# Kernel optimization log

Hardware: AMD Instinct MI355X
Metric: run time of the kernel (lower is better)

The kernel has to match this reference:

```python
import jax, jax.numpy as jnp
import numpy as np

C = 16       # celltypes
N = 20000    # nodes per PPI graph
D = 192      # in_channels == out_channels*heads (residual constraint)
H = 3        # node_heads
CO = 64      # out_channels per head
E = 320000   # edges per PPI graph
T = 32       # tissue nodes
K = 8        # neighbors per tissue
M = C + T    # metagraph nodes
R = 4        # metagraph relations
EM = 256     # edges per metagraph relation
S = 128      # sem_att_channels
TU = 100     # tissue_update iterations


def setup_inputs():
    key = jax.random.key(0)
    k = jax.random.split(key, 16)
    g = lambda kk, shp, sc: jax.random.normal(kk, shp, jnp.float32) * sc
    return {
        "ppi_x": g(k[0], (C, N, D), 1.0),
        "metagraph_x": g(k[1], (M, D), 1.0),
        "ppi_lin": g(k[2], (C, D, H * CO), 0.07),
        "ppi_att_src": g(k[3], (C, H, CO), 0.1),
        "ppi_att_dst": g(k[4], (C, H, CO), 0.1),
        "ppi_bias": jnp.zeros((C, H * CO), jnp.float32),
        "meta_lin": g(k[5], (R, H * CO, H * CO), 0.07),
        "meta_att_src": g(k[6], (R, H, CO), 0.1),
        "meta_att_dst": g(k[7], (R, H, CO), 0.1),
        "meta_bias": jnp.zeros((R, H * CO), jnp.float32),
        "W_sem": g(k[8], (H * CO, S), 0.08),
        "b_sem": jnp.zeros((S,), jnp.float32),
        "q_sem": g(k[9], (S,), 0.1),
        "ppi_edges": jax.random.randint(k[10], (C, 2, E), 0, N, dtype=jnp.int32),
        "meta_edges": jax.random.randint(k[11], (R, 2, EM), 0, M, dtype=jnp.int32),
        "tissue_nb": jax.random.randint(k[12], (T, K), 0, M, dtype=jnp.int32),
    }


def gat(x, lin, att_s, att_d, bias, edge, n):
    """PyG-style GATConv, concat heads. x:[n,Din], edge:[2,E] (src,dst)."""
    h = (x @ lin).reshape(n, H, CO)
    a_s = (h * att_s).sum(-1)   # [n,H]
    a_d = (h * att_d).sum(-1)
    src, dst = edge[0], edge[1]
    e = jax.nn.leaky_relu(a_s[src] + a_d[dst], negative_slope=0.2)  # [E,H]
    emax = jax.lax.stop_gradient(jax.ops.segment_max(e, dst, num_segments=n))
    emax = jnp.where(jnp.isfinite(emax), emax, 0.0)
    ex = jnp.exp(e - emax[dst])
    denom = jax.ops.segment_sum(ex, dst, num_segments=n)          # [n,H]
    out = jax.ops.segment_sum(ex[:, :, None] * h[src], dst, num_segments=n)
    out = out / jnp.where(denom > 0.0, denom, 1.0)[:, :, None]
    return out.reshape(n, H * CO) + bias


def sem_attention(out, W, b, q):
    """Semantic attention over relations. out:[M,R,Dh]."""
    w = jnp.tanh(jnp.einsum('mrd,ds->mrs', out, W) + b)
    beta = jax.nn.softmax(jnp.einsum('mrs,s->mr', w, q), axis=1)
    return jnp.einsum('mrd,mr->md', out, beta)


def forward(ppi_x, metagraph_x, ppi_lin, ppi_att_src, ppi_att_dst, ppi_bias,
            meta_lin, meta_att_src, meta_att_dst, meta_bias,
            W_sem, b_sem, q_sem, ppi_edges, meta_edges, tissue_nb):
    mx = metagraph_x
    # residual GAT per celltype, mean-pooled into the metagraph celltype row
    for c in range(C):
        att = ppi_x[c] + gat(ppi_x[c], ppi_lin[c], ppi_att_src[c], ppi_att_dst[c],
                             ppi_bias[c], ppi_edges[c], N)
        mx = mx.at[c].add(att.mean(0))
    # sequential (Gauss-Seidel) tissue-neighbor mean diffusion, TU sweeps
    def step(m, t):
        return m.at[C + t].set(m[tissue_nb[t]].mean(0)), None
    def sweep(m, _):
        m, _ = jax.lax.scan(step, m, jnp.arange(T))
        return m, None
    mx, _ = jax.lax.scan(sweep, mx, None, length=TU)
    # multi-relation metagraph GAT + semantic attention fusion
    outs = jnp.stack([gat(mx, meta_lin[r], meta_att_src[r], meta_att_dst[r],
                          meta_bias[r], meta_edges[r], M) for r in range(R)], axis=1)
    outs = jax.nn.relu(outs)  # torch applies relu after stacking
    return sem_attention(outs, W_sem, b_sem, q_sem)


def reference(ppi_x, metagraph_x, ppi_lin, ppi_att_src, ppi_att_dst, ppi_bias,
              meta_lin, meta_att_src, meta_att_dst, meta_bias,
              W_sem, b_sem, q_sem, ppi_edges, meta_edges, tissue_nb):
    return forward(ppi_x, metagraph_x, ppi_lin, ppi_att_src, ppi_att_dst, ppi_bias,
                   meta_lin, meta_att_src, meta_att_dst, meta_bias,
                   W_sem, b_sem, q_sem, ppi_edges, meta_edges, tissue_nb)
```

## Files before the change

kernel.cpp:

```cpp
#include <hip/hip_runtime.h>

#define CT 16
#define NN 20000
#define EE 320000
#define MM 48
#define RR 4
#define EMM 256
#define NRANGE 64
#define NPR 313
#define CAP 5632
#define MAGIC 13721941ULL

#define OFF_MEANX 0
#define OFF_P     3072
#define OFF_CNTD  12288
#define OFF_CNTS  13312
#define ZERO_FLOATS 14336
#define OFF_COMB  14336
#define OFF_AS    2574336
#define OFF_AD    3854336
#define OFF_U     5134336
#define OFF_V     5143552
#define OFF_MX    5152768
#define OFF_HH    5161984
#define OFF_OUTS  5198848
#define OFF_BIND  5235712
#define OFF_BINS  11002880
#define OFF_W     16770048
#define OFF_MX2   16772352

__device__ inline unsigned bucket_of(int d) {
    return (unsigned)(((unsigned long long)(unsigned)d * MAGIC) >> 32);
}

__global__ __launch_bounds__(192) void k_prep(const float* __restrict__ lin,
        const float* __restrict__ as_g, const float* __restrict__ ad_g,
        float* __restrict__ U, float* __restrict__ V, float* __restrict__ zws) {
    int c = blockIdx.x, d = threadIdx.x;
    int gt = c * 192 + d;
    for (int o = gt; o < ZERO_FLOATS; o += 16 * 192) zws[o] = 0.f;
    const float* L  = lin + ((size_t)c * 192 + d) * 192;
    const float* As = as_g + c * 192;
    const float* Ad = ad_g + c * 192;
#pragma unroll
    for (int h = 0; h < 3; ++h) {
        float u = 0.f, v = 0.f;
        for (int j = 0; j < 64; ++j) {
            float lv = L[h * 64 + j];
            u += lv * As[h * 64 + j];
            v += lv * Ad[h * 64 + j];
        }
        U[c * 576 + h * 192 + d] = u;
        V[c * 576 + h * 192 + d] = v;
    }
}

__global__ __launch_bounds__(256, 8) void k_front(const int* __restrict__ edges,
        int* __restrict__ cntD, int* __restrict__ cntS,
        int* __restrict__ binD, int* __restrict__ binS,
        const float* __restrict__ x, const float* __restrict__ U,
        const float* __restrict__ V, float* __restrict__ a_s,
        float* __restrict__ a_d, float* __restrict__ meanx,
        const int* __restrict__ nb, float* __restrict__ Wout) {
    __shared__ __align__(16) float smem[4608];
    int tid = threadIdx.x;
    if (blockIdx.x == 0) {
        float* B0 = smem;
        float* B1 = smem + 1536;
        float* B2 = smem + 3072;
        float* B[3] = {B0, B1, B2};
        for (int o = tid; o < 1536; o += 256) {
            int i = o / 48, j = o - i * 48;
            float idv = (j == 16 + i) ? 1.f : 0.f;
            B0[o] = idv;
            B1[o] = idv;
        }
        __syncthreads();
        if (tid < 48) {
            int j = tid;
            for (int t = 0; t < 32; ++t) {
                float acc = 0.f;
                for (int k = 0; k < 8; ++k) {
                    int idx = nb[t * 8 + k];
                    acc += (idx < 16) ? (j == idx ? 1.f : 0.f)
                                      : B0[(idx - 16) * 48 + j];
                }
                B0[t * 48 + j] = acc * 0.125f;
            }
        }
        __syncthreads();
        int iP = 0, iR = 1, iT = 2;
        int e = 100;
        while (e) {
            if (e & 1) {
                for (int o = tid; o < 1536; o += 256) {
                    int i = o / 48, j = o - i * 48;
                    float acc = (j < 16) ? B[iR][i * 48 + j] : 0.f;
                    for (int t = 0; t < 32; ++t)
                        acc += B[iR][i * 48 + 16 + t] * B[iP][t * 48 + j];
                    B[iT][o] = acc;
                }
                __syncthreads();
                int t_ = iR; iR = iT; iT = t_;
            }
            e >>= 1;
            if (e) {
                for (int o = tid; o < 1536; o += 256) {
                    int i = o / 48, j = o - i * 48;
                    float acc = (j < 16) ? B[iP][i * 48 + j] : 0.f;
                    for (int t = 0; t < 32; ++t)
                        acc += B[iP][i * 48 + 16 + t] * B[iP][t * 48 + j];
                    B[iT][o] = acc;
                }
                __syncthreads();
                int t_ = iP; iP = iT; iT = t_;
            }
        }
        for (int o = tid; o < 1536; o += 256) {
            int i = o / 48, j = o - i * 48;
            Wout[(16 + i) * 48 + j] = B[iR][o];
        }
    } else if (blockIdx.x < 1025) {
        int wg = blockIdx.x - 1;
        int ct = (wg & 7) * 2 + ((wg >> 3) & 1);
        int part = wg >> 4;
        int wave = tid >> 6;
        int* histD = (int*)smem;
        int* histS = histD + 256;
        int* curD  = histS + 256;
        int* curS  = curD + 64;
        if (tid < NRANGE) {
            histD[0 * 64 + tid] = 0; histD[1 * 64 + tid] = 0;
            histD[2 * 64 + tid] = 0; histD[3 * 64 + tid] = 0;
            histS[0 * 64 + tid] = 0; histS[1 * 64 + tid] = 0;
            histS[2 * 64 + tid] = 0; histS[3 * 64 + tid] = 0;
        }
        __syncthreads();
        const int* srcp = edges + (size_t)ct * 2 * EE;
        const int* dstp = srcp + EE;
        const int4* s4 = (const int4*)srcp;
        const int4* d4 = (const int4*)dstp;
        int base4 = part * 1250;
        for (int i = tid; i < 1250; i += 256) {
            int4 dv = d4[base4 + i];
            int4 sv = s4[base4 + i];
            atomicAdd(&histD[wave * 64 + bucket_of(dv.x)], 1);
            atomicAdd(&histD[wave * 64 + bucket_of(dv.y)], 1);
            atomicAdd(&histD[wave * 64 + bucket_of(dv.z)], 1);
            atomicAdd(&histD[wave * 64 + bucket_of(dv.w)], 1);
            atomicAdd(&histS[wave * 64 + bucket_of(sv.x)], 1);
            atomicAdd(&histS[wave * 64 + bucket_of(sv.y)], 1);
            atomicAdd(&histS[wave * 64 + bucket_of(sv.z)], 1);
            atomicAdd(&histS[wave * 64 + bucket_of(sv.w)], 1);
        }
        __syncthreads();
        if (tid < NRANGE) {
            int t = histD[tid] + histD[64 + tid] + histD[128 + tid] + histD[192 + tid];
            curD[tid] = atomicAdd(&cntD[ct * NRANGE + tid], t);
            int t2 = histS[tid] + histS[64 + tid] + histS[128 + tid] + histS[192 + tid];
            curS[tid] = atomicAdd(&cntS[ct * NRANGE + tid], t2);
        }
        __syncthreads();
        int* bD = binD + (size_t)ct * NRANGE * CAP;
        int* bS = binS + (size_t)ct * NRANGE * CAP;
#define EMIT2(ss, dd) { int pk = ((ss) << 15) | (dd); \
        unsigned bd = bucket_of(dd); int so = atomicAdd(&curD[bd], 1); \
        if (so < CAP) bD[bd * CAP + so] = pk; \
        unsigned bs = bucket_of(ss); int s2 = atomicAdd(&curS[bs], 1); \
        if (s2 < CAP) bS[bs * CAP + s2] = pk; }
        for (int i = tid; i < 1250; i += 256) {
            int4 dv = d4[base4 + i];
            int4 sv = s4[base4 + i];
            EMIT2(sv.x, dv.x); EMIT2(sv.y, dv.y); EMIT2(sv.z, dv.z); EMIT2(sv.w, dv.w);
        }
#undef EMIT2
    } else {
        int idx = blockIdx.x - 1025;
        int c = idx & 15;
        int start = (idx >> 4) * 160;
        int lane = tid & 63;
        int wave = tid >> 6;
        float* A = smem;
        float* blk = smem + 3264;
        if (tid < 192) blk[tid] = 0.f;
        float u0[3], u1[3], u2[3], v0[3], v1[3], v2[3];
#pragma unroll
        for (int h = 0; h < 3; ++h) {
            u0[h] = U[c * 576 + h * 192 + lane];
            u1[h] = U[c * 576 + h * 192 + 64 + lane];
            u2[h] = U[c * 576 + h * 192 + 128 + lane];
            v0[h] = V[c * 576 + h * 192 + lane];
            v1[h] = V[c * 576 + h * 192 + 64 + lane];
            v2[h] = V[c * 576 + h * 192 + 128 + lane];
        }
        __syncthreads();
        const float* xc = x + (size_t)c * NN * 192;
        float* asn = a_s + (size_t)c * NN * 4;
        float* adn = a_d + (size_t)c * NN * 4;
        float m0 = 0.f, m1 = 0.f, m2 = 0.f;
        float* Aa = A + (wave * 2) * 408;
        float* Ab = A + (wave * 2 + 1) * 408;
        int rrow = lane >> 3, seg = lane & 7;
        for (int i = 0; i < 20; ++i) {
            int na = start + wave + 8 * i;
            int nb_ = na + 4;
            const float* xa = xc + (size_t)na * 192;
            const float* xb = xc + (size_t)nb_ * 192;
            float xa0 = xa[lane], xa1 = xa[64 + lane], xa2 = xa[128 + lane];
            float xb0 = xb[lane], xb1 = xb[64 + lane], xb2 = xb[128 + lane];
            m0 += xa0 + xb0; m1 += xa1 + xb1; m2 += xa2 + xb2;
            Aa[0 * 68 + lane] = xa0 * u0[0] + xa1 * u1[0] + xa2 * u2[0];
            Aa[1 * 68 + lane] = xa0 * u0[1] + xa1 * u1[1] + xa2 * u2[1];
            Aa[2 * 68 + lane] = xa0 * u0[2] + xa1 * u1[2] + xa2 * u2[2];
            Aa[3 * 68 + lane] = xa0 * v0[0] + xa1 * v1[0] + xa2 * v2[0];
            Aa[4 * 68 + lane] = xa0 * v0[1] + xa1 * v1[1] + xa2 * v2[1];
            Aa[5 * 68 + lane] = xa0 * v0[2] + xa1 * v1[2] + xa2 * v2[2];
            Ab[0 * 68 + lane] = xb0 * u0[0] + xb1 * u1[0] + xb2 * u2[0];
            Ab[1 * 68 + lane] = xb0 * u0[1] + xb1 * u1[1] + xb2 * u2[1];
            Ab[2 * 68 + lane] = xb0 * u0[2] + xb1 * u1[2] + xb2 * u2[2];
            Ab[3 * 68 + lane] = xb0 * v0[0] + xb1 * v1[0] + xb2 * v2[0];
            Ab[4 * 68 + lane] = xb0 * v0[1] + xb1 * v1[1] + xb2 * v2[1];
            Ab[5 * 68 + lane] = xb0 * v0[2] + xb1 * v1[2] + xb2 * v2[2];
            float sa = 0.f, sb = 0.f;
            if (lane < 48) {
                const float4* pa = (const float4*)(Aa + rrow * 68 + seg * 8);
                const float4* pb = (const float4*)(Ab + rrow * 68 + seg * 8);
                float4 a0 = pa[0], a1 = pa[1];
                float4 b0 = pb[0], b1 = pb[1];
                sa = ((a0.x + a0.y) + (a0.z + a0.w)) + ((a1.x + a1.y) + (a1.z + a1.w));
                sb = ((b0.x + b0.y) + (b0.z + b0.w)) + ((b1.x + b1.y) + (b1.z + b1.w));
            }
            sa += __shfl_xor(sa, 1, 64); sb += __shfl_xor(sb, 1, 64);
            sa += __shfl_xor(sa, 2, 64); sb += __shfl_xor(sb, 2, 64);
            sa += __shfl_xor(sa, 4, 64); sb += __shfl_xor(sb, 4, 64);
            if (lane < 48 && seg == 0) {
                if (rrow < 3) { asn[na * 4 + rrow] = sa;      asn[nb_ * 4 + rrow] = sb; }
                else          { adn[na * 4 + rrow - 3] = sa;  adn[nb_ * 4 + rrow - 3] = sb; }
            }
        }
        atomicAdd(&blk[lane], m0);
        atomicAdd(&blk[64 + lane], m1);
        atomicAdd(&blk[128 + lane], m2);
        __syncthreads();
        if (tid < 192) atomicAdd(&meanx[c * 192 + tid], blk[tid]);
    }
}

__device__ inline void map_ct(int wg, int& ct, int& j) {
    int xcd = wg & 7;
    ct = xcd * 2 + ((wg >> 3) & 1);
    j = wg >> 4;
}

__global__ __launch_bounds__(512) void k_eden_b(const int* __restrict__ bin,
        const int* __restrict__ cnt, const float* __restrict__ a_s,
        const float* __restrict__ a_d, float* __restrict__ comb) {
    int ct, bkt;
    map_ct(blockIdx.x, ct, bkt);
    int lo = bkt * NPR;
    int nnode = NN - lo < NPR ? NN - lo : NPR;
    int tid = threadIdx.x;
    __shared__ float adl[NPR * 3];
    __shared__ float den[NPR * 3];
    const float4* as4 = (const float4*)(a_s + (size_t)ct * NN * 4);
    const float4* ad4 = (const float4*)(a_d + (size_t)ct * NN * 4);
    for (int m = tid; m < nnode; m += 512) {
        float4 v = ad4[lo + m];
        adl[m * 3] = v.x; adl[m * 3 + 1] = v.y; adl[m * 3 + 2] = v.z;
    }
    for (int o = tid; o < nnode * 3; o += 512) den[o] = 0.f;
    __syncthreads();
    int n = cnt[ct * NRANGE + bkt]; if (n > CAP) n = CAP;
    const int* bc = bin + ((size_t)ct * NRANGE + bkt) * CAP;
    for (int i = tid; i < n; i += 512) {
        int v = bc[i];
        int d = v & 32767, s = v >> 15;
        int dl = d - lo;
        float4 av = as4[s];
        float e0 = av.x + adl[dl * 3];     e0 = e0 >= 0.f ? e0 : 0.2f * e0;
        float e1 = av.y + adl[dl * 3 + 1]; e1 = e1 >= 0.f ? e1 : 0.2f * e1;
        float e2 = av.z + adl[dl * 3 + 2]; e2 = e2 >= 0.f ? e2 : 0.2f * e2;
        atomicAdd(&den[dl * 3],     __expf(e0));
        atomicAdd(&den[dl * 3 + 1], __expf(e1));
        atomicAdd(&den[dl * 3 + 2], __expf(e2));
    }
    __syncthreads();
    float4* cb = (float4*)(comb + (size_t)ct * NN * 8);
    for (int m = tid; m < nnode; m += 512) {
        float d0 = den[m * 3], d1 = den[m * 3 + 1], d2 = den[m * 3 + 2];
        float4 a, b;
        a.x = adl[m * 3]; a.y = adl[m * 3 + 1]; a.z = adl[m * 3 + 2]; a.w = 0.f;
        b.x = d0 > 0.f ? 1.f / d0 : 0.f;
        b.y = d1 > 0.f ? 1.f / d1 : 0.f;
        b.z = d2 > 0.f ? 1.f / d2 : 0.f;
        b.w = 0.f;
        cb[(size_t)(lo + m) * 2]     = a;
        cb[(size_t)(lo + m) * 2 + 1] = b;
    }
}

__global__ __launch_bounds__(512) void k_es_p(const int* __restrict__ bin,
        const int* __restrict__ cnt, const float* __restrict__ a_s,
        const float* __restrict__ comb, const float* __restrict__ x,
        float* __restrict__ p) {
    int ct, bkt;
    map_ct(blockIdx.x, ct, bkt);
    int lo = bkt * NPR;
    int nnode = NN - lo < NPR ? NN - lo : NPR;
    int tid = threadIdx.x;
    __shared__ float asl[NPR * 3];
    __shared__ float sl[NPR * 3];
    __shared__ float blk[576];
    const float4* as4 = (const float4*)(a_s + (size_t)ct * NN * 4);
    const float4* cb  = (const float4*)(comb + (size_t)ct * NN * 8);
    for (int m = tid; m < nnode; m += 512) {
        float4 v = as4[lo + m];
        asl[m * 3] = v.x; asl[m * 3 + 1] = v.y; asl[m * 3 + 2] = v.z;
    }
    for (int o = tid; o < nnode * 3; o += 512) sl[o] = 0.f;
    for (int o = tid; o < 576; o += 512) blk[o] = 0.f;
    __syncthreads();
    int n = cnt[ct * NRANGE + bkt]; if (n > CAP) n = CAP;
    const int* bc = bin + ((size_t)ct * NRANGE + bkt) * CAP;
    for (int i = tid; i < n; i += 512) {
        int v = bc[i];
        int d = v & 32767, s = v >> 15;
        int slc = s - lo;
        float4 av = cb[(size_t)d * 2];
        float4 dv = cb[(size_t)d * 2 + 1];
        float e0 = asl[slc * 3]     + av.x; e0 = e0 >= 0.f ? e0 : 0.2f * e0;
        float e1 = asl[slc * 3 + 1] + av.y; e1 = e1 >= 0.f ? e1 : 0.2f * e1;
        float e2 = asl[slc * 3 + 2] + av.z; e2 = e2 >= 0.f ? e2 : 0.2f * e2;
        atomicAdd(&sl[slc * 3],     __expf(e0) * dv.x);
        atomicAdd(&sl[slc * 3 + 1], __expf(e1) * dv.y);
        atomicAdd(&sl[slc * 3 + 2], __expf(e2) * dv.z);
    }
    __syncthreads();
    int lane = tid & 63;
    int wave = tid >> 6;
    const float* xc = x + (size_t)ct * NN * 192;
    float a00 = 0, a01 = 0, a02 = 0, a10 = 0, a11 = 0, a12 = 0, a20 = 0, a21 = 0, a22 = 0;
    for (int m = wave; m < nnode; m += 8) {
        float s0 = sl[m * 3], s1 = sl[m * 3 + 1], s2 = sl[m * 3 + 2];
        const float* xr = xc + (size_t)(lo + m) * 192;
        float x0 = xr[lane], x1 = xr[64 + lane], x2 = xr[128 + lane];
        a00 += s0 * x0; a01 += s0 * x1; a02 += s0 * x2;
        a10 += s1 * x0; a11 += s1 * x1; a12 += s1 * x2;
        a20 += s2 * x0; a21 += s2 * x1; a22 += s2 * x2;
    }
    atomicAdd(&blk[0 * 192 + lane], a00);
    atomicAdd(&blk[0 * 192 + 64 + lane], a01);
    atomicAdd(&blk[0 * 192 + 128 + lane], a02);
    atomicAdd(&blk[1 * 192 + lane], a10);
    atomicAdd(&blk[1 * 192 + 64 + lane], a11);
    atomicAdd(&blk[1 * 192 + 128 + lane], a12);
    atomicAdd(&blk[2 * 192 + lane], a20);
    atomicAdd(&blk[2 * 192 + 64 + lane], a21);
    atomicAdd(&blk[2 * 192 + 128 + lane], a22);
    __syncthreads();
    for (int o = tid; o < 576; o += 512) atomicAdd(&p[ct * 576 + o], blk[o]);
}

__global__ __launch_bounds__(192) void k_mx(const float* __restrict__ mgx,
        const float* __restrict__ meanx, const float* __restrict__ p,
        const float* __restrict__ lin, const float* __restrict__ bias,
        float* __restrict__ mx) {
    int m = blockIdx.x, j = threadIdx.x;
    if (m < CT) {
        int h = j >> 6;
        const float* ph = p + m * 576 + h * 192;
        const float* L = lin + (size_t)m * 36864;
        float acc = 0.f;
        for (int k = 0; k < 192; ++k) acc += ph[k] * L[k * 192 + j];
        mx[m * 192 + j] = mgx[m * 192 + j] + (meanx[m * 192 + j] + acc) * (1.f / NN)
                          + bias[m * 192 + j];
    } else {
        mx[m * 192 + j] = mgx[m * 192 + j];
    }
}

__global__ __launch_bounds__(192) void k_tapply(const float* __restrict__ W,
        const float* __restrict__ mx, float* __restrict__ mx2) {
    int m = blockIdx.x, j = threadIdx.x;
    if (m < CT) {
        mx2[m * 192 + j] = mx[m * 192 + j];
    } else {
        float acc = 0.f;
        for (int k = 0; k < 48; ++k) acc += W[m * 48 + k] * mx[k * 192 + j];
        mx2[m * 192 + j] = acc;
    }
}

__global__ __launch_bounds__(192) void k_meta_h(const float* __restrict__ mx,
        const float* __restrict__ lin, float* __restrict__ hh) {
    int r = blockIdx.x, m = blockIdx.y, j = threadIdx.x;
    const float* L = lin + (size_t)r * 36864;
    const float* xr = mx + m * 192;
    float acc = 0.f;
    for (int k = 0; k < 192; ++k) acc += xr[k] * L[k * 192 + j];
    hh[((size_t)r * 48 + m) * 192 + j] = acc;
}

__global__ __launch_bounds__(256) void k_meta_edge(const float* __restrict__ hh,
        const float* __restrict__ att_s, const float* __restrict__ att_d,
        const float* __restrict__ bias, const int* __restrict__ edges,
        float* __restrict__ outs) {
    int r = blockIdx.x;
    int tid = threadIdx.x;
    __shared__ float as_[48][3], ad_[48][3], den[48][3];
    const float* hr = hh + (size_t)r * 48 * 192;
    float* og = outs + (size_t)r * 48 * 192;
    if (tid < 144) {
        int m = tid / 3, h = tid % 3;
        const float* As = att_s + r * 192 + h * 64;
        const float* Ad = att_d + r * 192 + h * 64;
        float s_ = 0.f, d_ = 0.f;
        for (int j = 0; j < 64; ++j) {
            float hv = hr[m * 192 + h * 64 + j];
            s_ += hv * As[j]; d_ += hv * Ad[j];
        }
        as_[m][h] = s_; ad_[m][h] = d_;
        den[m][h] = 0.f;
    }
    for (int o = tid; o < 9216; o += 256) og[o] = bias[r * 192 + (o % 192)];
    __syncthreads();
    int s = edges[(size_t)r * 2 * EMM + tid];
    int d = edges[(size_t)r * 2 * EMM + EMM + tid];
    float e0 = as_[s][0] + ad_[d][0]; e0 = e0 >= 0.f ? e0 : 0.2f * e0;
    float e1 = as_[s][1] + ad_[d][1]; e1 = e1 >= 0.f ? e1 : 0.2f * e1;
    float e2 = as_[s][2] + ad_[d][2]; e2 = e2 >= 0.f ? e2 : 0.2f * e2;
    float ex0 = __expf(e0), ex1 = __expf(e1), ex2 = __expf(e2);
    atomicAdd(&den[d][0], ex0);
    atomicAdd(&den[d][1], ex1);
    atomicAdd(&den[d][2], ex2);
    __syncthreads();
    float w0 = ex0 / den[d][0], w1 = ex1 / den[d][1], w2 = ex2 / den[d][2];
    const float* hs = hr + s * 192;
    float* od = og + d * 192;
    for (int j = 0; j < 64; ++j)        atomicAdd(&od[j], w0 * hs[j]);
    for (int j = 64; j < 128; ++j)      atomicAdd(&od[j], w1 * hs[j]);
    for (int j = 128; j < 192; ++j)     atomicAdd(&od[j], w2 * hs[j]);
}

__global__ __launch_bounds__(128) void k_sem(const float* __restrict__ outs,
        const float* __restrict__ W, const float* __restrict__ b,
        const float* __restrict__ q, float* __restrict__ out) {
    int m = blockIdx.x, s = threadIdx.x;
    __shared__ float ro[4][192];
    __shared__ float red[4][128];
    __shared__ float beta[4];
    for (int o = s; o < 768; o += 128) {
        int r = o / 192, d = o - r * 192;
        float v = outs[((size_t)r * 48 + m) * 192 + d];
        ro[r][d] = v > 0.f ? v : 0.f;
    }
    __syncthreads();
    float p0 = 0, p1 = 0, p2 = 0, p3 = 0;
    for (int d = 0; d < 192; ++d) {
        float wv = W[d * 128 + s];
        p0 += ro[0][d] * wv; p1 += ro[1][d] * wv; p2 += ro[2][d] * wv; p3 += ro[3][d] * wv;
    }
    float bb = b[s], qq = q[s];
    red[0][s] = tanhf(p0 + bb) * qq;
    red[1][s] = tanhf(p1 + bb) * qq;
    red[2][s] = tanhf(p2 + bb) * qq;
    red[3][s] = tanhf(p3 + bb) * qq;
    __syncthreads();
    for (int off = 64; off >= 1; off >>= 1) {
        if (s < off) {
            red[0][s] += red[0][s + off];
            red[1][s] += red[1][s + off];
            red[2][s] += red[2][s + off];
            red[3][s] += red[3][s + off];
        }
        __syncthreads();
    }
    if (s == 0) {
        float s0 = red[0][0], s1 = red[1][0], s2 = red[2][0], s3 = red[3][0];
        float mx4 = fmaxf(fmaxf(s0, s1), fmaxf(s2, s3));
        float e0 = __expf(s0 - mx4), e1 = __expf(s1 - mx4);
        float e2 = __expf(s2 - mx4), e3 = __expf(s3 - mx4);
        float inv = 1.f / (e0 + e1 + e2 + e3);
        beta[0] = e0 * inv; beta[1] = e1 * inv; beta[2] = e2 * inv; beta[3] = e3 * inv;
    }
    __syncthreads();
    for (int d = s; d < 192; d += 128) {
        float acc = ro[0][d] * beta[0] + ro[1][d] * beta[1]
                  + ro[2][d] * beta[2] + ro[3][d] * beta[3];
        out[m * 192 + d] = acc;
    }
}

extern "C" void kernel_launch(void* const* d_in, const int* in_sizes, int n_in,
                              void* d_out, int out_size, void* d_ws, size_t ws_size,
                              hipStream_t stream) {
    const float* ppi_x    = (const float*)d_in[0];
    const float* mgx      = (const float*)d_in[1];
    const float* ppi_lin  = (const float*)d_in[2];
    const float* ppi_as   = (const float*)d_in[3];
    const float* ppi_ad   = (const float*)d_in[4];
    const float* ppi_b    = (const float*)d_in[5];
    const float* meta_lin = (const float*)d_in[6];
    const float* meta_as  = (const float*)d_in[7];
    const float* meta_ad  = (const float*)d_in[8];
    const float* meta_b   = (const float*)d_in[9];
    const float* W_sem    = (const float*)d_in[10];
    const float* b_sem    = (const float*)d_in[11];
    const float* q_sem    = (const float*)d_in[12];
    const int*   ppi_e    = (const int*)d_in[13];
    const int*   meta_e   = (const int*)d_in[14];
    const int*   tnb      = (const int*)d_in[15];

    float* ws   = (float*)d_ws;
    float* mnx  = ws + OFF_MEANX;
    float* pac  = ws + OFF_P;
    int*   cntD = (int*)(ws + OFF_CNTD);
    int*   cntS = (int*)(ws + OFF_CNTS);
    float* comb = ws + OFF_COMB;
    float* a_s  = ws + OFF_AS;
    float* a_d  = ws + OFF_AD;
    float* U    = ws + OFF_U;
    float* V    = ws + OFF_V;
    float* mx   = ws + OFF_MX;
    float* hh   = ws + OFF_HH;
    float* outs = ws + OFF_OUTS;
    int*   binD = (int*)(ws + OFF_BIND);
    int*   binS = (int*)(ws + OFF_BINS);
    float* Wt   = ws + OFF_W;
    float* mx2  = ws + OFF_MX2;

    k_prep<<<16, 192, 0, stream>>>(ppi_lin, ppi_as, ppi_ad, U, V, ws);
    k_front<<<3025, 256, 0, stream>>>(ppi_e, cntD, cntS, binD, binS,
                                      ppi_x, U, V, a_s, a_d, mnx, tnb, Wt);
    k_eden_b<<<1024, 512, 0, stream>>>(binD, cntD, a_s, a_d, comb);
    k_es_p<<<1024, 512, 0, stream>>>(binS, cntS, a_s, comb, ppi_x, pac);
    k_mx<<<48, 192, 0, stream>>>(mgx, mnx, pac, ppi_lin, ppi_b, mx);
    k_tapply<<<48, 192, 0, stream>>>(Wt, mx, mx2);
    k_meta_h<<<dim3(4, 48), 192, 0, stream>>>(mx2, meta_lin, hh);
    k_meta_edge<<<4, 256, 0, stream>>>(hh, meta_as, meta_ad, meta_b, meta_e, outs);
    k_sem<<<48, 128, 0, stream>>>(outs, W_sem, b_sem, q_sem, (float*)d_out);
}
```

Before: 500.1 us.

## Bin edges by 2D source-destination cells to localize source gathers

```diff
diff --git a/kernel.cpp b/kernel.cpp
--- a/kernel.cpp
+++ b/kernel.cpp
@@ -6,31 +6,39 @@
 #define MM 48
 #define RR 4
 #define EMM 256
-#define NRANGE 64
-#define NPR 313
-#define CAP 5632
-#define MAGIC 13721941ULL
+#define NSB 32
+#define NPRS 625
+#define NDB 64
+#define NPRD 313
+#define CELLS 2048
+#define CAP2 240
+#define CAPS 11008
+#define MAGICS 6871948ULL
+#define MAGICD 13721941ULL
 
 #define OFF_MEANX 0
 #define OFF_P     3072
-#define OFF_CNTD  12288
-#define OFF_CNTS  13312
-#define ZERO_FLOATS 14336
-#define OFF_COMB  14336
-#define OFF_AS    2574336
-#define OFF_AD    3854336
-#define OFF_U     5134336
-#define OFF_V     5143552
-#define OFF_MX    5152768
-#define OFF_HH    5161984
-#define OFF_OUTS  5198848
-#define OFF_BIND  5235712
-#define OFF_BINS  11002880
-#define OFF_W     16770048
-#define OFF_MX2   16772352
-
-__device__ inline unsigned bucket_of(int d) {
-    return (unsigned)(((unsigned long long)(unsigned)d * MAGIC) >> 32);
+#define OFF_CNT2  12288
+#define OFF_CNTS  45056
+#define ZERO_FLOATS 45568
+#define OFF_COMB  45568
+#define OFF_AS    2605568
+#define OFF_AD    3885568
+#define OFF_U     5165568
+#define OFF_V     5174784
+#define OFF_MX    5184000
+#define OFF_HH    5193216
+#define OFF_OUTS  5230080
+#define OFF_W     5266944
+#define OFF_MX2   5269248
+#define OFF_BIN2  5278464
+#define OFF_BINS  13142784
+
+__device__ inline unsigned bucket_s(int v) {
+    return (unsigned)(((unsigned long long)(unsigned)v * MAGICS) >> 32);
+}
+__device__ inline unsigned bucket_d(int v) {
+    return (unsigned)(((unsigned long long)(unsigned)v * MAGICD) >> 32);
 }
 
 __global__ __launch_bounds__(192) void k_prep(const float* __restrict__ lin,
@@ -56,8 +64,8 @@
 }
 
 __global__ __launch_bounds__(256, 8) void k_front(const int* __restrict__ edges,
-        int* __restrict__ cntD, int* __restrict__ cntS,
-        int* __restrict__ binD, int* __restrict__ binS,
+        int* __restrict__ cnt2, int* __restrict__ cntS,
+        int* __restrict__ bin2, int* __restrict__ binS,
         const float* __restrict__ x, const float* __restrict__ U,
         const float* __restrict__ V, float* __restrict__ a_s,
         float* __restrict__ a_d, float* __restrict__ meanx,
@@ -124,56 +132,51 @@
         int wg = blockIdx.x - 1;
         int ct = (wg & 7) * 2 + ((wg >> 3) & 1);
         int part = wg >> 4;
-        int wave = tid >> 6;
-        int* histD = (int*)smem;
-        int* histS = histD + 256;
-        int* curD  = histS + 256;
-        int* curS  = curD + 64;
-        if (tid < NRANGE) {
-            histD[0 * 64 + tid] = 0; histD[1 * 64 + tid] = 0;
-            histD[2 * 64 + tid] = 0; histD[3 * 64 + tid] = 0;
-            histS[0 * 64 + tid] = 0; histS[1 * 64 + tid] = 0;
-            histS[2 * 64 + tid] = 0; histS[3 * 64 + tid] = 0;
-        }
+        int* hist  = (int*)smem;
+        int* cur   = hist + 2048;
+        int* histS = cur + 2048;
+        int* curS  = histS + 32;
+        for (int o = tid; o < 2048; o += 256) hist[o] = 0;
+        if (tid < NSB) histS[tid] = 0;
         __syncthreads();
         const int* srcp = edges + (size_t)ct * 2 * EE;
         const int* dstp = srcp + EE;
         const int4* s4 = (const int4*)srcp;
         const int4* d4 = (const int4*)dstp;
         int base4 = part * 1250;
+#define CELL_OF(ss, dd) ((int)(bucket_s(ss) * NDB + bucket_d(dd)))
         for (int i = tid; i < 1250; i += 256) {
             int4 dv = d4[base4 + i];
             int4 sv = s4[base4 + i];
-            atomicAdd(&histD[wave * 64 + bucket_of(dv.x)], 1);
-            atomicAdd(&histD[wave * 64 + bucket_of(dv.y)], 1);
-            atomicAdd(&histD[wave * 64 + bucket_of(dv.z)], 1);
-            atomicAdd(&histD[wave * 64 + bucket_of(dv.w)], 1);
-            atomicAdd(&histS[wave * 64 + bucket_of(sv.x)], 1);
-            atomicAdd(&histS[wave * 64 + bucket_of(sv.y)], 1);
-            atomicAdd(&histS[wave * 64 + bucket_of(sv.z)], 1);
-            atomicAdd(&histS[wave * 64 + bucket_of(sv.w)], 1);
-        }
-        __syncthreads();
-        if (tid < NRANGE) {
-            int t = histD[tid] + histD[64 + tid] + histD[128 + tid] + histD[192 + tid];
-            curD[tid] = atomicAdd(&cntD[ct * NRANGE + tid], t);
-            int t2 = histS[tid] + histS[64 + tid] + histS[128 + tid] + histS[192 + tid];
-            curS[tid] = atomicAdd(&cntS[ct * NRANGE + tid], t2);
-        }
-        __syncthreads();
-        int* bD = binD + (size_t)ct * NRANGE * CAP;
-        int* bS = binS + (size_t)ct * NRANGE * CAP;
-#define EMIT2(ss, dd) { int pk = ((ss) << 15) | (dd); \
-        unsigned bd = bucket_of(dd); int so = atomicAdd(&curD[bd], 1); \
-        if (so < CAP) bD[bd * CAP + so] = pk; \
-        unsigned bs = bucket_of(ss); int s2 = atomicAdd(&curS[bs], 1); \
-        if (s2 < CAP) bS[bs * CAP + s2] = pk; }
+            atomicAdd(&hist[CELL_OF(sv.x, dv.x)], 1);
+            atomicAdd(&hist[CELL_OF(sv.y, dv.y)], 1);
+            atomicAdd(&hist[CELL_OF(sv.z, dv.z)], 1);
+            atomicAdd(&hist[CELL_OF(sv.w, dv.w)], 1);
+            atomicAdd(&histS[bucket_s(sv.x)], 1);
+            atomicAdd(&histS[bucket_s(sv.y)], 1);
+            atomicAdd(&histS[bucket_s(sv.z)], 1);
+            atomicAdd(&histS[bucket_s(sv.w)], 1);
+        }
+        __syncthreads();
+        for (int c = tid; c < 2048; c += 256)
+            cur[c] = atomicAdd(&cnt2[ct * CELLS + c], hist[c]);
+        if (tid < NSB) curS[tid] = atomicAdd(&cntS[ct * NSB + tid], histS[tid]);
+        __syncthreads();
+        int* b2 = bin2 + (size_t)ct * CELLS * CAP2;
+        int* bS = binS + (size_t)ct * NSB * CAPS;
+#define EMIT3(ss, dd) { int pk = ((ss) << 15) | (dd); \
+        int cell = CELL_OF(ss, dd); \
+        int so = atomicAdd(&cur[cell], 1); \
+        if (so < CAP2) b2[cell * CAP2 + so] = pk; \
+        unsigned bs = bucket_s(ss); int s2 = atomicAdd(&curS[bs], 1); \
+        if (s2 < CAPS) bS[bs * CAPS + s2] = pk; }
         for (int i = tid; i < 1250; i += 256) {
             int4 dv = d4[base4 + i];
             int4 sv = s4[base4 + i];
-            EMIT2(sv.x, dv.x); EMIT2(sv.y, dv.y); EMIT2(sv.z, dv.z); EMIT2(sv.w, dv.w);
-        }
-#undef EMIT2
+            EMIT3(sv.x, dv.x); EMIT3(sv.y, dv.y); EMIT3(sv.z, dv.z); EMIT3(sv.w, dv.w);
+        }
+#undef EMIT3
+#undef CELL_OF
     } else {
         int idx = blockIdx.x - 1025;
         int c = idx & 15;
@@ -252,16 +255,18 @@
     j = wg >> 4;
 }
 
-__global__ __launch_bounds__(512) void k_eden_b(const int* __restrict__ bin,
-        const int* __restrict__ cnt, const float* __restrict__ a_s,
+__global__ __launch_bounds__(512) void k_eden_b(const int* __restrict__ bin2,
+        const int* __restrict__ cnt2, const float* __restrict__ a_s,
         const float* __restrict__ a_d, float* __restrict__ comb) {
-    int ct, bkt;
-    map_ct(blockIdx.x, ct, bkt);
-    int lo = bkt * NPR;
-    int nnode = NN - lo < NPR ? NN - lo : NPR;
+    int ct, db;
+    map_ct(blockIdx.x, ct, db);
+    int lo = db * NPRD;
+    int nnode = NN - lo < NPRD ? NN - lo : NPRD;
     int tid = threadIdx.x;
-    __shared__ float adl[NPR * 3];
-    __shared__ float den[NPR * 3];
+    __shared__ float asl[2500 * 3];
+    __shared__ float adl[NPRD * 3];
+    __shared__ float den[NPRD * 3];
+    __shared__ int   pfx[5];
     const float4* as4 = (const float4*)(a_s + (size_t)ct * NN * 4);
     const float4* ad4 = (const float4*)(a_d + (size_t)ct * NN * 4);
     for (int m = tid; m < nnode; m += 512) {
@@ -269,20 +274,41 @@
         adl[m * 3] = v.x; adl[m * 3 + 1] = v.y; adl[m * 3 + 2] = v.z;
     }
     for (int o = tid; o < nnode * 3; o += 512) den[o] = 0.f;
-    __syncthreads();
-    int n = cnt[ct * NRANGE + bkt]; if (n > CAP) n = CAP;
-    const int* bc = bin + ((size_t)ct * NRANGE + bkt) * CAP;
-    for (int i = tid; i < n; i += 512) {
-        int v = bc[i];
-        int d = v & 32767, s = v >> 15;
-        int dl = d - lo;
-        float4 av = as4[s];
-        float e0 = av.x + adl[dl * 3];     e0 = e0 >= 0.f ? e0 : 0.2f * e0;
-        float e1 = av.y + adl[dl * 3 + 1]; e1 = e1 >= 0.f ? e1 : 0.2f * e1;
-        float e2 = av.z + adl[dl * 3 + 2]; e2 = e2 >= 0.f ? e2 : 0.2f * e2;
-        atomicAdd(&den[dl * 3],     __expf(e0));
-        atomicAdd(&den[dl * 3 + 1], __expf(e1));
-        atomicAdd(&den[dl * 3 + 2], __expf(e2));
+    const int* c2 = cnt2 + ct * CELLS;
+    const int* b2 = bin2 + (size_t)ct * CELLS * CAP2;
+    for (int g = 0; g < 8; ++g) {
+        int nbase = g * 2500;
+        __syncthreads();
+        for (int m = tid; m < 2500; m += 512) {
+            float4 v = as4[nbase + m];
+            asl[m * 3] = v.x; asl[m * 3 + 1] = v.y; asl[m * 3 + 2] = v.z;
+        }
+        if (tid == 0) {
+            int acc = 0;
+            pfx[0] = 0;
+            for (int k = 0; k < 4; ++k) {
+                int c = c2[(g * 4 + k) * NDB + db];
+                if (c > CAP2) c = CAP2;
+                acc += c;
+                pfx[k + 1] = acc;
+            }
+        }
+        __syncthreads();
+        int total = pfx[4];
+        int p1 = pfx[1], p2 = pfx[2], p3 = pfx[3];
+        for (int i = tid; i < total; i += 512) {
+            int k = (i >= p1) + (i >= p2) + (i >= p3);
+            int j = i - pfx[k];
+            int v = b2[((g * 4 + k) * NDB + db) * CAP2 + j];
+            int sg = (v >> 15) - nbase;
+            int dl = (v & 32767) - lo;
+            float e0 = asl[sg * 3]     + adl[dl * 3];     e0 = e0 >= 0.f ? e0 : 0.2f * e0;
+            float e1 = asl[sg * 3 + 1] + adl[dl * 3 + 1]; e1 = e1 >= 0.f ? e1 : 0.2f * e1;
+            float e2 = asl[sg * 3 + 2] + adl[dl * 3 + 2]; e2 = e2 >= 0.f ? e2 : 0.2f * e2;
+            atomicAdd(&den[dl * 3],     __expf(e0));
+            atomicAdd(&den[dl * 3 + 1], __expf(e1));
+            atomicAdd(&den[dl * 3 + 2], __expf(e2));
+        }
     }
     __syncthreads();
     float4* cb = (float4*)(comb + (size_t)ct * NN * 8);
@@ -303,29 +329,28 @@
         const int* __restrict__ cnt, const float* __restrict__ a_s,
         const float* __restrict__ comb, const float* __restrict__ x,
         float* __restrict__ p) {
-    int ct, bkt;
-    map_ct(blockIdx.x, ct, bkt);
-    int lo = bkt * NPR;
-    int nnode = NN - lo < NPR ? NN - lo : NPR;
+    int ct, sb;
+    map_ct(blockIdx.x, ct, sb);
+    int lo = sb * NPRS;
     int tid = threadIdx.x;
-    __shared__ float asl[NPR * 3];
-    __shared__ float sl[NPR * 3];
+    __shared__ float asl[NPRS * 3];
+    __shared__ float sl[NPRS * 3];
     __shared__ float blk[576];
     const float4* as4 = (const float4*)(a_s + (size_t)ct * NN * 4);
     const float4* cb  = (const float4*)(comb + (size_t)ct * NN * 8);
-    for (int m = tid; m < nnode; m += 512) {
+    for (int m = tid; m < NPRS; m += 512) {
         float4 v = as4[lo + m];
         asl[m * 3] = v.x; asl[m * 3 + 1] = v.y; asl[m * 3 + 2] = v.z;
     }
-    for (int o = tid; o < nnode * 3; o += 512) sl[o] = 0.f;
+    for (int o = tid; o < NPRS * 3; o += 512) sl[o] = 0.f;
     for (int o = tid; o < 576; o += 512) blk[o] = 0.f;
     __syncthreads();
-    int n = cnt[ct * NRANGE + bkt]; if (n > CAP) n = CAP;
-    const int* bc = bin + ((size_t)ct * NRANGE + bkt) * CAP;
+    int n = cnt[ct * NSB + sb]; if (n > CAPS) n = CAPS;
+    const int* bc = bin + ((size_t)ct * NSB + sb) * CAPS;
     for (int i = tid; i < n; i += 512) {
         int v = bc[i];
-        int d = v & 32767, s = v >> 15;
-        int slc = s - lo;
+        int d = v & 32767;
+        int slc = (v >> 15) - lo;
         float4 av = cb[(size_t)d * 2];
         float4 dv = cb[(size_t)d * 2 + 1];
         float e0 = asl[slc * 3]     + av.x; e0 = e0 >= 0.f ? e0 : 0.2f * e0;
@@ -340,7 +365,7 @@
     int wave = tid >> 6;
     const float* xc = x + (size_t)ct * NN * 192;
     float a00 = 0, a01 = 0, a02 = 0, a10 = 0, a11 = 0, a12 = 0, a20 = 0, a21 = 0, a22 = 0;
-    for (int m = wave; m < nnode; m += 8) {
+    for (int m = wave; m < NPRS; m += 8) {
         float s0 = sl[m * 3], s1 = sl[m * 3 + 1], s2 = sl[m * 3 + 2];
         const float* xr = xc + (size_t)(lo + m) * 192;
         float x0 = xr[lane], x1 = xr[64 + lane], x2 = xr[128 + lane];
@@ -514,7 +539,7 @@
     float* ws   = (float*)d_ws;
     float* mnx  = ws + OFF_MEANX;
     float* pac  = ws + OFF_P;
-    int*   cntD = (int*)(ws + OFF_CNTD);
+    int*   cnt2 = (int*)(ws + OFF_CNT2);
     int*   cntS = (int*)(ws + OFF_CNTS);
     float* comb = ws + OFF_COMB;
     float* a_s  = ws + OFF_AS;
@@ -524,16 +549,16 @@
     float* mx   = ws + OFF_MX;
     float* hh   = ws + OFF_HH;
     float* outs = ws + OFF_OUTS;
-    int*   binD = (int*)(ws + OFF_BIND);
-    int*   binS = (int*)(ws + OFF_BINS);
     float* Wt   = ws + OFF_W;
     float* mx2  = ws + OFF_MX2;
+    int*   bin2 = (int*)(ws + OFF_BIN2);
+    int*   binS = (int*)(ws + OFF_BINS);
 
     k_prep<<<16, 192, 0, stream>>>(ppi_lin, ppi_as, ppi_ad, U, V, ws);
-    k_front<<<3025, 256, 0, stream>>>(ppi_e, cntD, cntS, binD, binS,
+    k_front<<<3025, 256, 0, stream>>>(ppi_e, cnt2, cntS, bin2, binS,
                                       ppi_x, U, V, a_s, a_d, mnx, tnb, Wt);
-    k_eden_b<<<1024, 512, 0, stream>>>(binD, cntD, a_s, a_d, comb);
-    k_es_p<<<1024, 512, 0, stream>>>(binS, cntS, a_s, comb, ppi_x, pac);
+    k_eden_b<<<1024, 512, 0, stream>>>(bin2, cnt2, a_s, a_d, comb);
+    k_es_p<<<512, 512, 0, stream>>>(binS, cntS, a_s, comb, ppi_x, pac);
     k_mx<<<48, 192, 0, stream>>>(mgx, mnx, pac, ppi_lin, ppi_b, mx);
     k_tapply<<<48, 192, 0, stream>>>(Wt, mx, mx2);
     k_meta_h<<<dim3(4, 48), 192, 0, stream>>>(mx2, meta_lin, hh);
```

New measurement: 539.0 us. 7.8% more time.
